# Optimization experiments

Hardware: AMD Instinct MI355X
Metric: run time of the kernel (lower is better)

Reference implementation:

```python
import jax, jax.numpy as jnp
import numpy as np

N = 100000        # nodes
E = 1600000       # edges (nnz per Laplacian order)
K_ORDERS = 3      # K + 1
IN_C = 64
OUT_C = 64


def setup_inputs() -> dict:
    key = jax.random.key(0)
    ks = jax.random.split(key, 7)
    X_real = jax.random.normal(ks[0], (N, IN_C), jnp.float32)
    X_imag = jax.random.normal(ks[1], (N, IN_C), jnp.float32)
    edge_index = jax.random.randint(ks[2], (2, E), 0, N)  # [rows; cols]
    L_real_vals = jax.random.normal(ks[3], (K_ORDERS, E), jnp.float32) * 0.1
    L_imag_vals = jax.random.normal(ks[4], (K_ORDERS, E), jnp.float32) * 0.1
    stdv = 1.0 / np.sqrt(OUT_C)
    weight = jax.random.uniform(ks[5], (K_ORDERS, IN_C, OUT_C), jnp.float32, -stdv, stdv)
    bias = jnp.zeros((1, OUT_C), jnp.float32)
    return {"X_real": X_real, "X_imag": X_imag, "edge_index": edge_index,
            "L_real_vals": L_real_vals, "L_imag_vals": L_imag_vals,
            "weight": weight, "bias": bias}


def _spmm(vals, rows, cols, X):
    # y[i] = sum_{(i,j) in edges} vals_ij * X[j]   (equivalent to torch.spmm)
    return jax.ops.segment_sum(vals[:, None] * X[cols], rows, num_segments=N)


def reference(X_real, X_imag, edge_index, L_real_vals, L_imag_vals, weight, bias):
    rows, cols = edge_index[0], edge_index[1]
    real = jnp.zeros((N, OUT_C), X_real.dtype)
    imag = jnp.zeros((N, OUT_C), X_real.dtype)
    for k in range(K_ORDERS):  # small fixed number of spectral orders
        ArXr = _spmm(L_real_vals[k], rows, cols, X_real)
        AiXi = _spmm(L_imag_vals[k], rows, cols, X_imag)
        AiXr = _spmm(L_imag_vals[k], rows, cols, X_real)
        ArXi = _spmm(L_real_vals[k], rows, cols, X_imag)
        real = real + (ArXr - AiXi) @ weight[k]
        imag = imag + (AiXr + ArXi) @ weight[k]
    return real + bias, imag + bias
```

## Files before the change

### kernel.cpp

```cpp
#include <hip/hip_runtime.h>
#include <hip/hip_fp16.h>


constexpr int N_NODES = 100000;
constexpr int E_EDGES = 1600000;
constexpr int CH = 64;
constexpr int NP = 100096;
constexpr int NBUCK = NP / 256;
constexpr int CHUNK_A = 2048;
constexpr int NBLK_A = (E_EDGES + CHUNK_A - 1) / CHUNK_A;
constexpr unsigned COLMASK = 0x1FFFFu;

typedef unsigned u32x4 __attribute__((ext_vector_type(4)));
typedef _Float16 h2f __attribute__((ext_vector_type(2)));
typedef _Float16 h8f __attribute__((ext_vector_type(8)));
typedef float f32x4 __attribute__((ext_vector_type(4)));

__device__ __forceinline__ float fdot2h(unsigned a, unsigned b, float c) {
#if __has_builtin(__builtin_amdgcn_fdot2)
    return __builtin_amdgcn_fdot2(__builtin_bit_cast(h2f, a),
                                  __builtin_bit_cast(h2f, b), c, false);
#else
    float2 af = __half22float2(__builtin_bit_cast(__half2, a));
    float2 bf = __half22float2(__builtin_bit_cast(__half2, b));
    return c + af.x * bf.x + af.y * bf.y;
#endif
}

__device__ __forceinline__ unsigned pack2(float a, float b) {
    return __builtin_bit_cast(unsigned, __floats2half2_rn(a, b));
}

__device__ __forceinline__ unsigned rot16(unsigned u) {
    return (u >> 16) | (u << 16);
}

__global__ __launch_bounds__(256) void init_out_kernel(const float* __restrict__ bias,
                                                       float* __restrict__ out) {
    int i = blockIdx.x * 256 + threadIdx.x;
    out[i] = bias[i & 63];
}

__global__ __launch_bounds__(1024) void prep_hist_kernel(const float* __restrict__ Xr,
                                                         const float* __restrict__ Xi,
                                                         const int* __restrict__ rows,
                                                         unsigned* __restrict__ Xh,
                                                         int* __restrict__ bcnt) {
    __shared__ int lh[NBUCK];
    const int tid = threadIdx.x;
    for (int t = tid; t < NBUCK; t += 1024) lh[t] = 0;
    __syncthreads();
    const int base = blockIdx.x * CHUNK_A;
#pragma unroll
    for (int h = 0; h < 2; ++h) {
        const int i = base + h * 1024 + tid;
        if (i < E_EDGES) {
            const float4 r = ((const float4*)Xr)[i];
            const float4 m = ((const float4*)Xi)[i];
            uint4 u;
            u.x = pack2(r.x, m.x);
            u.y = pack2(r.y, m.y);
            u.z = pack2(r.z, m.z);
            u.w = pack2(r.w, m.w);
            ((uint4*)Xh)[i] = u;
            atomicAdd(&lh[rows[i] >> 8], 1);
        }
    }
    __syncthreads();
    for (int t = tid; t < NBUCK; t += 1024)
        if (lh[t]) atomicAdd(&bcnt[t], lh[t]);
}

__global__ __launch_bounds__(512) void cscan_kernel(const int* __restrict__ bcnt,
                                                    int* __restrict__ cofs,
                                                    int* __restrict__ ccur,
                                                    const float* __restrict__ W,
                                                    h8f* __restrict__ Bpack) {
    __shared__ int s[512];
    const int t = threadIdx.x;
    int v = (t < NBUCK) ? bcnt[t] : 0;
    s[t] = v;
    __syncthreads();
    for (int off = 1; off < 512; off <<= 1) {
        int a = (t >= off) ? s[t - off] : 0;
        __syncthreads();
        s[t] += a;
        __syncthreads();
    }
    if (t < NBUCK) {
        cofs[t] = s[t] - v;
        ccur[t] = s[t] - v;
    }
    if (t == NBUCK - 1) cofs[NBUCK] = s[t];

    for (int sidx = t; sidx < 24 * 64; sidx += 512) {
        const int L = sidx & 63;
        const int ntkc = sidx >> 6;
        const int nt = ntkc & 3;
        const int kc = ntkc >> 2;
        const int colb = nt * 16 + (L & 15);
        const int kbase = kc * 32 + ((L >> 4) << 3);
        h8f vv;
#pragma unroll
        for (int j = 0; j < 8; ++j) vv[j] = (_Float16)W[(kbase + j) * 64 + colb];
        Bpack[sidx] = vv;
    }
}

__global__ __launch_bounds__(1024) void partA_kernel(const int* __restrict__ rows,
                                                     const int* __restrict__ cols,
                                                     const float* __restrict__ Lr,
                                                     const float* __restrict__ Li,
                                                     int* __restrict__ ccur,
                                                     u32x4* __restrict__ temp) {
    __shared__ u32x4 sRec[CHUNK_A];
    __shared__ int sDst[CHUNK_A];
    __shared__ int lh[NBUCK];
    __shared__ int lcur[NBUCK];
    __shared__ int gdel[NBUCK];
    __shared__ int ss[512];
    const int tid = threadIdx.x;
    const int base = blockIdx.x * CHUNK_A;
    const int nedge = min(CHUNK_A, E_EDGES - base);

    for (int t = tid; t < NBUCK; t += 1024) lh[t] = 0;
    __syncthreads();
    for (int j = tid; j < nedge; j += 1024) atomicAdd(&lh[rows[base + j] >> 8], 1);
    __syncthreads();

    if (tid < 512) ss[tid] = (tid < NBUCK) ? lh[tid] : 0;
    __syncthreads();
    for (int off = 1; off < 512; off <<= 1) {
        int a = 0;
        if (tid < 512 && tid >= off) a = ss[tid - off];
        __syncthreads();
        if (tid < 512) ss[tid] += a;
        __syncthreads();
    }
    if (tid < NBUCK) {
        const int excl = ss[tid] - lh[tid];
        lcur[tid] = excl;
        const int gb = lh[tid] ? atomicAdd(&ccur[tid], lh[tid]) : 0;
        gdel[tid] = gb - excl;
    }
    __syncthreads();

    for (int j = tid; j < nedge; j += 1024) {
        const int e = base + j;
        const int r = rows[e];
        const int bk = r >> 8;
        const int pos = atomicAdd(&lcur[bk], 1);
        u32x4 u;
        u.x = (unsigned)cols[e] | ((unsigned)(r & 255) << 17);
        u.y = pack2(Lr[e], Li[e]);
        u.z = pack2(Lr[E_EDGES + e], Li[E_EDGES + e]);
        u.w = pack2(Lr[2 * E_EDGES + e], Li[2 * E_EDGES + e]);
        sRec[pos] = u;
        sDst[pos] = gdel[bk] + pos;
    }
    __syncthreads();

    for (int c = tid; c < nedge; c += 1024) temp[sDst[c]] = sRec[c];
}

__global__ __launch_bounds__(1024) void partB_kernel(const int* __restrict__ cofs,
                                                     const u32x4* __restrict__ temp,
                                                     u32x4* __restrict__ payload,
                                                     int* __restrict__ rowst) {
    const int b = blockIdx.x;
    const int t = threadIdx.x;
    const int start = cofs[b];
    const int endp = cofs[b + 1];
    __shared__ int lh[256];
    __shared__ int s[256];
    if (t < 256) lh[t] = 0;
    __syncthreads();
    for (int i = start + t; i < endp; i += 1024)
        atomicAdd(&lh[temp[i].x >> 17], 1);
    __syncthreads();
    int v = 0;
    if (t < 256) {
        v = lh[t];
        s[t] = v;
    }
    __syncthreads();
    for (int off = 1; off < 256; off <<= 1) {
        int a = (t >= off && t < 256) ? s[t - off] : 0;
        __syncthreads();
        if (t < 256) s[t] += a;
        __syncthreads();
    }
    if (t < 256) {
        const int excl = s[t] - v;
        rowst[b * 256 + t] = start + excl;
        lh[t] = excl;
    }
    if (b == NBUCK - 1 && t == 0) rowst[NBUCK * 256] = endp;
    __syncthreads();
    for (int i = start + t; i < endp; i += 1024) {
        u32x4 q = temp[i];
        const int rl = (int)(q.x >> 17);
        const int pos = start + atomicAdd(&lh[rl], 1);
        payload[pos] = q;
    }
}

__global__ __launch_bounds__(256) void row6_kernel(const int* __restrict__ rowst,
                                                   const u32x4* __restrict__ payload,
                                                   const unsigned* __restrict__ Xh,
                                                   const h8f* __restrict__ Bpack,
                                                   const float* __restrict__ bias,
                                                   float* __restrict__ out) {
    __shared__ __half sY[2][16][200];
    const int w = (int)threadIdx.x >> 6;
    const int lane = threadIdx.x & 63;
    const int band = blockIdx.x * 16;

    for (int q = 0; q < 4; ++q) {
        const int ri = w * 4 + q;
        const int r = __builtin_amdgcn_readfirstlane(band + ri);
        const int start = rowst[r];
        const int end = rowst[r + 1];
        const int n = end - start;

        float aR0 = 0.f, aI0 = 0.f, aR1 = 0.f, aI1 = 0.f, aR2 = 0.f, aI2 = 0.f;

        auto gx = [&](unsigned cw) -> unsigned {
            return Xh[(size_t)(cw & COLMASK) * 64 + lane];
        };
        auto accum = [&](const u32x4& qq, unsigned xv) {
            aR0 = fdot2h(qq.y ^ 0x80000000u, xv, aR0);
            aI0 = fdot2h(rot16(qq.y), xv, aI0);
            aR1 = fdot2h(qq.z ^ 0x80000000u, xv, aR1);
            aI1 = fdot2h(rot16(qq.z), xv, aI1);
            aR2 = fdot2h(qq.w ^ 0x80000000u, xv, aR2);
            aI2 = fdot2h(rot16(qq.w), xv, aI2);
        };

        if (n >= 12) {
            int p = start;
            u32x4 P0 = payload[p], P1 = payload[p + 1], P2 = payload[p + 2],
                  P3 = payload[p + 3], P4 = payload[p + 4], P5 = payload[p + 5],
                  P6 = payload[p + 6], P7 = payload[p + 7];
            unsigned x0 = gx(P0.x), x1 = gx(P1.x), x2 = gx(P2.x), x3 = gx(P3.x);
            unsigned x4 = gx(P4.x), x5 = gx(P5.x), x6 = gx(P6.x), x7 = gx(P7.x);

            for (; p + 11 < end; p += 4) {
                u32x4 Q0 = payload[p + 8], Q1 = payload[p + 9];
                u32x4 Q2 = payload[p + 10], Q3 = payload[p + 11];
                accum(P0, x0);
                accum(P1, x1);
                accum(P2, x2);
                accum(P3, x3);
                P0 = P4; P1 = P5; P2 = P6; P3 = P7;
                x0 = x4; x1 = x5; x2 = x6; x3 = x7;
                P4 = Q0; P5 = Q1; P6 = Q2; P7 = Q3;
                x4 = gx(P4.x);
                x5 = gx(P5.x);
                x6 = gx(P6.x);
                x7 = gx(P7.x);
            }
            accum(P0, x0);
            accum(P1, x1);
            accum(P2, x2);
            accum(P3, x3);
            accum(P4, x4);
            accum(P5, x5);
            accum(P6, x6);
            accum(P7, x7);
            for (p += 8; p < end; ++p) {
                u32x4 qq = payload[p];
                unsigned xv = gx(qq.x);
                accum(qq, xv);
            }
        } else {
            for (int p = start; p < end; ++p) {
                u32x4 qq = payload[p];
                unsigned xv = gx(qq.x);
                accum(qq, xv);
            }
        }

        sY[0][ri][lane] = __float2half(aR0);
        sY[0][ri][64 + lane] = __float2half(aR1);
        sY[0][ri][128 + lane] = __float2half(aR2);
        sY[1][ri][lane] = __float2half(aI0);
        sY[1][ri][64 + lane] = __float2half(aI1);
        sY[1][ri][128 + lane] = __float2half(aI2);
    }
    __syncthreads();

    const int nt = w;
    const int m = lane & 15;
    const int ko = (lane >> 4) << 3;
    f32x4 accR = (f32x4){0.f, 0.f, 0.f, 0.f};
    f32x4 accI = (f32x4){0.f, 0.f, 0.f, 0.f};
#pragma unroll
    for (int kc = 0; kc < 6; ++kc) {
        h8f bf = Bpack[(kc * 4 + nt) * 64 + lane];
        h8f aR = *(const h8f*)&sY[0][m][kc * 32 + ko];
        h8f aI = *(const h8f*)&sY[1][m][kc * 32 + ko];
        accR = __builtin_amdgcn_mfma_f32_16x16x32_f16(aR, bf, accR, 0, 0, 0);
        accI = __builtin_amdgcn_mfma_f32_16x16x32_f16(aI, bf, accI, 0, 0, 0);
    }
    const int colw = lane & 15;
    const int rbase = (lane >> 4) << 2;
    const float b = bias[nt * 16 + colw];
#pragma unroll
    for (int rr = 0; rr < 4; ++rr) {
        const int row = band + rbase + rr;
        __builtin_nontemporal_store(accR[rr] + b,
                                    &out[(size_t)row * 64 + nt * 16 + colw]);
        __builtin_nontemporal_store(accI[rr] + b,
                                    &out[(size_t)(N_NODES + row) * 64 + nt * 16 + colw]);
    }
}

template <int NK>
__global__ __launch_bounds__(256) void xw_kernel(const float* __restrict__ Xr,
                                                 const float* __restrict__ Xi,
                                                 const float* __restrict__ W,
                                                 __half2* __restrict__ XWh) {
    __shared__ float sW[NK][64][64];
    __shared__ float4 sX4[2][32][16];
    const int tid = threadIdx.x;

    float4* swf = (float4*)&sW[0][0][0];
    const float4* gW = (const float4*)W;
    for (int i = tid; i < NK * 1024; i += 256) swf[i] = gW[i];

    const int rowbase = blockIdx.x * 32;
    float4* sxf = (float4*)sX4;
    const float4* gXr = (const float4*)(Xr + (size_t)rowbase * CH);
    const float4* gXi = (const float4*)(Xi + (size_t)rowbase * CH);
    for (int i = tid; i < 512; i += 256) {
        sxf[i] = gXr[i];
        sxf[512 + i] = gXi[i];
    }
    __syncthreads();

    const int col = tid & 63;
    const int rg = tid >> 6;

    float acc[8][2 * NK];
#pragma unroll
    for (int i = 0; i < 8; ++i)
#pragma unroll
        for (int c2 = 0; c2 < 2 * NK; ++c2) acc[i][c2] = 0.0f;

#pragma unroll 2
    for (int j4 = 0; j4 < 16; ++j4) {
        float w[NK][4];
#pragma unroll
        for (int k = 0; k < NK; ++k)
#pragma unroll
            for (int jj = 0; jj < 4; ++jj) w[k][jj] = sW[k][j4 * 4 + jj][col];
#pragma unroll
        for (int i = 0; i < 8; ++i) {
            float4 xr = sX4[0][rg * 8 + i][j4];
            float4 xi = sX4[1][rg * 8 + i][j4];
            const float xra[4] = {xr.x, xr.y, xr.z, xr.w};
            const float xia[4] = {xi.x, xi.y, xi.z, xi.w};
#pragma unroll
            for (int jj = 0; jj < 4; ++jj)
#pragma unroll
                for (int k = 0; k < NK; ++k) {
                    acc[i][2 * k] += xra[jj] * w[k][jj];
                    acc[i][2 * k + 1] += xia[jj] * w[k][jj];
                }
        }
    }

#pragma unroll
    for (int i = 0; i < 8; ++i) {
        __half2* dst = XWh + (size_t)(rowbase + rg * 8 + i) * (NK * 64);
#pragma unroll
        for (int k = 0; k < NK; ++k)
            dst[k * 64 + col] = __floats2half2_rn(acc[i][2 * k], acc[i][2 * k + 1]);
    }
}

template <int NK>
__global__ __launch_bounds__(256) void edge_kernel(const int* __restrict__ rows,
                                                   const int* __restrict__ cols,
                                                   const float* __restrict__ Lr,
                                                   const float* __restrict__ Li,
                                                   const __half2* __restrict__ XWh,
                                                   float* __restrict__ out) {
    const int gid = blockIdx.x * 256 + threadIdx.x;
    const int e = gid >> 6;
    const int lane = gid & 63;
    if (e >= E_EDGES) return;

    const int row = rows[e];
    const int colN = cols[e];
    const __half2* xw = XWh + (size_t)colN * (NK * 64);

    float rc = 0.0f, ic = 0.0f;
#pragma unroll
    for (int k = 0; k < NK; ++k) {
        const float lr = Lr[(size_t)k * E_EDGES + e];
        const float li = Li[(size_t)k * E_EDGES + e];
        float2 v = __half22float2(xw[k * 64 + lane]);
        rc += lr * v.x - li * v.y;
        ic += li * v.x + lr * v.y;
    }
    unsafeAtomicAdd(out + (size_t)row * 64 + lane, rc);
    unsafeAtomicAdd(out + ((size_t)N_NODES + row) * 64 + lane, ic);
}

extern "C" void kernel_launch(void* const* d_in, const int* in_sizes, int n_in,
                              void* d_out, int out_size, void* d_ws, size_t ws_size,
                              hipStream_t stream) {
    const float* Xr = (const float*)d_in[0];
    const float* Xi = (const float*)d_in[1];
    const int* ei = (const int*)d_in[2];
    const float* Lr = (const float*)d_in[3];
    const float* Li = (const float*)d_in[4];
    const float* W = (const float*)d_in[5];
    const float* bias = (const float*)d_in[6];
    float* out = (float*)d_out;

    const int* rows = ei;
    const int* cols = ei + E_EDGES;

    char* wsb = (char*)d_ws;
    const int edge_grid = (int)((size_t)E_EDGES * 64 / 256);
    const int gemm_grid = N_NODES / 32;

    unsigned* Xh = (unsigned*)wsb;
    unsigned* payload = (unsigned*)(wsb + 25600000);
    u32x4* temp = (u32x4*)(wsb + 51200000);
    int* rowst = (int*)(wsb + 76800000);
    int* bcnt = (int*)(wsb + 77204480);
    int* cofs = (int*)(wsb + 77206080);
    int* ccur = (int*)(wsb + 77207680);
    h8f* Bpack = (h8f*)(wsb + 77209280);
    const size_t need_new = 77233856;

    if (ws_size >= need_new) {
        hipMemsetAsync(bcnt, 0, NBUCK * sizeof(int), stream);
        prep_hist_kernel<<<NBLK_A, 1024, 0, stream>>>(Xr, Xi, rows, Xh, bcnt);
        cscan_kernel<<<1, 512, 0, stream>>>(bcnt, cofs, ccur, W, Bpack);
        partA_kernel<<<NBLK_A, 1024, 0, stream>>>(rows, cols, Lr, Li, ccur, temp);
        partB_kernel<<<NBUCK, 1024, 0, stream>>>(cofs, temp, (u32x4*)payload, rowst);
        row6_kernel<<<N_NODES / 16, 256, 0, stream>>>(rowst, (const u32x4*)payload, Xh,
                                                      Bpack, bias, out);
        return;
    }

    __half2* XWh = (__half2*)wsb;
    const size_t need_onepass = 76800000;

    if (ws_size >= need_onepass) {
        init_out_kernel<<<2 * N_NODES * CH / 256, 256, 0, stream>>>(bias, out);
        xw_kernel<3><<<gemm_grid, 256, 0, stream>>>(Xr, Xi, W, XWh);
        edge_kernel<3><<<edge_grid, 256, 0, stream>>>(rows, cols, Lr, Li, XWh, out);
    } else {
        init_out_kernel<<<2 * N_NODES * CH / 256, 256, 0, stream>>>(bias, out);
        for (int k = 0; k < 3; ++k) {
            xw_kernel<1><<<gemm_grid, 256, 0, stream>>>(Xr, Xi, W + (size_t)k * 4096, XWh);
            edge_kernel<1><<<edge_grid, 256, 0, stream>>>(rows, cols,
                                                          Lr + (size_t)k * E_EDGES,
                                                          Li + (size_t)k * E_EDGES, XWh, out);
        }
    }
}
```

Measured before the change: 156.6 us.

## Store per-block bucket histograms and compute deterministic offsets via column scan

```diff
diff --git a/kernel.cpp b/kernel.cpp
--- a/kernel.cpp
+++ b/kernel.cpp
@@ -45,7 +45,8 @@
                                                          const float* __restrict__ Xi,
                                                          const int* __restrict__ rows,
                                                          unsigned* __restrict__ Xh,
-                                                         int* __restrict__ bcnt) {
+                                                         int* __restrict__ bcnt,
+                                                         int* __restrict__ bhist) {
     __shared__ int lh[NBUCK];
     const int tid = threadIdx.x;
     for (int t = tid; t < NBUCK; t += 1024) lh[t] = 0;
@@ -67,13 +68,15 @@
         }
     }
     __syncthreads();
-    for (int t = tid; t < NBUCK; t += 1024)
-        if (lh[t]) atomicAdd(&bcnt[t], lh[t]);
+    for (int t = tid; t < NBUCK; t += 1024) {
+        const int c = lh[t];
+        bhist[(size_t)blockIdx.x * NBUCK + t] = c;
+        if (c) atomicAdd(&bcnt[t], c);
+    }
 }
 
 __global__ __launch_bounds__(512) void cscan_kernel(const int* __restrict__ bcnt,
                                                     int* __restrict__ cofs,
-                                                    int* __restrict__ ccur,
                                                     const float* __restrict__ W,
                                                     h8f* __restrict__ Bpack) {
     __shared__ int s[512];
@@ -87,10 +90,7 @@
         s[t] += a;
         __syncthreads();
     }
-    if (t < NBUCK) {
-        cofs[t] = s[t] - v;
-        ccur[t] = s[t] - v;
-    }
+    if (t < NBUCK) cofs[t] = s[t] - v;
     if (t == NBUCK - 1) cofs[NBUCK] = s[t];
 
     for (int sidx = t; sidx < 24 * 64; sidx += 512) {
@@ -107,11 +107,39 @@
     }
 }
 
+__global__ __launch_bounds__(256) void colscan_kernel(const int* __restrict__ cofs,
+                                                      const int* __restrict__ bhist,
+                                                      int* __restrict__ bofs) {
+    const int b = blockIdx.x;
+    const int t = threadIdx.x;
+    __shared__ int s[256];
+    __shared__ int carry;
+    if (t == 0) carry = cofs[b];
+    __syncthreads();
+    for (int base = 0; base < NBLK_A; base += 256) {
+        const int idx = base + t;
+        int v = (idx < NBLK_A) ? bhist[(size_t)idx * NBUCK + b] : 0;
+        s[t] = v;
+        __syncthreads();
+        for (int off = 1; off < 256; off <<= 1) {
+            int a = (t >= off) ? s[t - off] : 0;
+            __syncthreads();
+            s[t] += a;
+            __syncthreads();
+        }
+        if (idx < NBLK_A) bofs[(size_t)idx * NBUCK + b] = carry + s[t] - v;
+        __syncthreads();
+        if (t == 255) carry += s[255];
+        __syncthreads();
+    }
+}
+
 __global__ __launch_bounds__(1024) void partA_kernel(const int* __restrict__ rows,
                                                      const int* __restrict__ cols,
                                                      const float* __restrict__ Lr,
                                                      const float* __restrict__ Li,
-                                                     int* __restrict__ ccur,
+                                                     const int* __restrict__ bhist,
+                                                     const int* __restrict__ bofs,
                                                      u32x4* __restrict__ temp) {
     __shared__ u32x4 sRec[CHUNK_A];
     __shared__ int sDst[CHUNK_A];
@@ -123,11 +151,8 @@
     const int base = blockIdx.x * CHUNK_A;
     const int nedge = min(CHUNK_A, E_EDGES - base);
 
-    for (int t = tid; t < NBUCK; t += 1024) lh[t] = 0;
-    __syncthreads();
-    for (int j = tid; j < nedge; j += 1024) atomicAdd(&lh[rows[base + j] >> 8], 1);
-    __syncthreads();
-
+    if (tid < NBUCK) lh[tid] = bhist[(size_t)blockIdx.x * NBUCK + tid];
+    __syncthreads();
     if (tid < 512) ss[tid] = (tid < NBUCK) ? lh[tid] : 0;
     __syncthreads();
     for (int off = 1; off < 512; off <<= 1) {
@@ -140,8 +165,7 @@
     if (tid < NBUCK) {
         const int excl = ss[tid] - lh[tid];
         lcur[tid] = excl;
-        const int gb = lh[tid] ? atomicAdd(&ccur[tid], lh[tid]) : 0;
-        gdel[tid] = gb - excl;
+        gdel[tid] = bofs[(size_t)blockIdx.x * NBUCK + tid] - excl;
     }
     __syncthreads();
 
@@ -434,15 +458,17 @@
     int* rowst = (int*)(wsb + 76800000);
     int* bcnt = (int*)(wsb + 77204480);
     int* cofs = (int*)(wsb + 77206080);
-    int* ccur = (int*)(wsb + 77207680);
-    h8f* Bpack = (h8f*)(wsb + 77209280);
-    const size_t need_new = 77233856;
+    h8f* Bpack = (h8f*)(wsb + 77207680);
+    int* bhist = (int*)(wsb + 77232256);
+    int* bofs = (int*)(wsb + 78455424);
+    const size_t need_new = 79678592;
 
     if (ws_size >= need_new) {
         hipMemsetAsync(bcnt, 0, NBUCK * sizeof(int), stream);
-        prep_hist_kernel<<<NBLK_A, 1024, 0, stream>>>(Xr, Xi, rows, Xh, bcnt);
-        cscan_kernel<<<1, 512, 0, stream>>>(bcnt, cofs, ccur, W, Bpack);
-        partA_kernel<<<NBLK_A, 1024, 0, stream>>>(rows, cols, Lr, Li, ccur, temp);
+        prep_hist_kernel<<<NBLK_A, 1024, 0, stream>>>(Xr, Xi, rows, Xh, bcnt, bhist);
+        cscan_kernel<<<1, 512, 0, stream>>>(bcnt, cofs, W, Bpack);
+        colscan_kernel<<<NBUCK, 256, 0, stream>>>(cofs, bhist, bofs);
+        partA_kernel<<<NBLK_A, 1024, 0, stream>>>(rows, cols, Lr, Li, bhist, bofs, temp);
         partB_kernel<<<NBUCK, 1024, 0, stream>>>(cofs, temp, (u32x4*)payload, rowst);
         row6_kernel<<<N_NODES / 16, 256, 0, stream>>>(rowst, (const u32x4*)payload, Xh,
                                                       Bpack, bias, out);
```

After: 156.1 us. No clear change (-0.3%).
